# Performance work log

Measured on AMD Instinct MI355X. Metric: run time of the kernel, lower is better.

Reference implementation:

```python
import jax, jax.numpy as jnp
import numpy as np

H = 1024  # hidden_features
I = 64    # input_dims
O = 2     # output_dims
T = 4096  # timesteps


def setup_inputs() -> dict:
    key = jax.random.key(0)
    ks = jax.random.split(key, 12)
    s = 1.0 / np.sqrt(H)  # torch LSTMCell/Linear init scale
    return {
        "x_in":  jax.random.normal(ks[0], (T, I), dtype=jnp.float32),
        "W_ih1": jax.random.uniform(ks[1], (4 * H, I), jnp.float32, -s, s),
        "W_hh1": jax.random.uniform(ks[2], (4 * H, H), jnp.float32, -s, s),
        "b_ih1": jax.random.uniform(ks[3], (4 * H,), jnp.float32, -s, s),
        "b_hh1": jax.random.uniform(ks[4], (4 * H,), jnp.float32, -s, s),
        "W_ih2": jax.random.uniform(ks[5], (4 * H, H), jnp.float32, -s, s),
        "W_hh2": jax.random.uniform(ks[6], (4 * H, H), jnp.float32, -s, s),
        "b_ih2": jax.random.uniform(ks[7], (4 * H,), jnp.float32, -s, s),
        "b_hh2": jax.random.uniform(ks[8], (4 * H,), jnp.float32, -s, s),
        "W_out": jax.random.uniform(ks[9], (O, H), jnp.float32, -s, s),
        "b_out": jax.random.uniform(ks[10], (O,), jnp.float32, -s, s),
    }


def _lstm_cell(x, h, c, W_ih, W_hh, b_ih, b_hh):
    # PyTorch LSTMCell gate order: i, f, g, o
    gates = x @ W_ih.T + b_ih + h @ W_hh.T + b_hh  # [4H]
    i, f, g, o = jnp.split(gates, 4)
    i = jax.nn.sigmoid(i)
    f = jax.nn.sigmoid(f)
    g = jnp.tanh(g)
    o = jax.nn.sigmoid(o)
    c_new = f * c + i * g
    h_new = o * jnp.tanh(c_new)
    return h_new, c_new


def reference(x_in, W_ih1, W_hh1, b_ih1, b_hh1,
              W_ih2, W_hh2, b_ih2, b_hh2, W_out, b_out):
    def step(carry, x_t):
        h1, c1, h2, c2 = carry
        h1, c1 = _lstm_cell(x_t, h1, c1, W_ih1, W_hh1, b_ih1, b_hh1)
        h2, c2 = _lstm_cell(h1, h2, c2, W_ih2, W_hh2, b_ih2, b_hh2)
        out = h2 @ W_out.T + b_out  # [O]
        return (h1, c1, h2, c2), out

    z = jnp.zeros((H,), dtype=x_in.dtype)
    init = (z, z, z, z)
    _, outputs = jax.lax.scan(step, init, x_in)  # outputs: [T, O]
    return outputs
```

## Files before the change

### kernel.cpp

```cpp
#include <hip/hip_runtime.h>
#include <math.h>


#define HID 1024
#define DIN 64
#define TSTEPS 4096
#define NWG 256
#define TPB 512

typedef unsigned long long u64;
typedef unsigned int u32;

#define H2_OFF 2048
#define WS_NEED_U64 (2048ull + 4097ull * 1024ull)
#define WS_NEED_BYTES (WS_NEED_U64 * 8ull)
#define WS_ZERO_BYTES 32768

#define WLDS_F4 (16 * 512)
#define DYN_LDS_BYTES (WLDS_F4 * 16 + 2 * 1152 * 4)

__device__ __forceinline__ float sigmoid_f(float v) {
    return 1.0f / (1.0f + __expf(-v));
}
__device__ __forceinline__ float tanh_f(float v) {
    return 2.0f / (1.0f + __expf(-2.0f * v)) - 1.0f;
}

__device__ __forceinline__ void st_pair(u64* p, float h, u32 tag) {
    u64 pk = ((u64)tag << 32) | (u64)__float_as_uint(h);
    __hip_atomic_store(p, pk, __ATOMIC_RELAXED, __HIP_MEMORY_SCOPE_AGENT);
}
__device__ __forceinline__ u64 ld_pair(const u64* p) {
    return __hip_atomic_load(p, __ATOMIC_RELAXED, __HIP_MEMORY_SCOPE_AGENT);
}
#define PTAG(v) ((u32)((v) >> 32))
#define PVAL(v) (__uint_as_float((u32)(v)))

#define PIN4(v) asm volatile("" : "+v"((v).x), "+v"((v).y), "+v"((v).z), "+v"((v).w))
#define PIN_W1() do { \
    PIN4(w1a); PIN4(w1b); PIN4(w1c); PIN4(w1d); \
    PIN4(w1e); PIN4(w1f); PIN4(w1g); PIN4(w1h); \
} while (0)

#define ASTEP(j, W1) do {                                           \
    float4 hv = *(const float4*)(hb + 4*(j));                       \
    float4 w2 = wlds[(j)*512 + tid];                                \
    a0 = fmaf((W1).x, hv.x, a0); a1 = fmaf((W1).y, hv.y, a1);       \
    a2 = fmaf((W1).z, hv.z, a2); a3 = fmaf((W1).w, hv.w, a3);       \
    e0 = fmaf(w2.x, hv.x, e0); e1 = fmaf(w2.y, hv.y, e1);           \
    e2 = fmaf(w2.z, hv.z, e2); e3 = fmaf(w2.w, hv.w, e3);           \
} while (0)

#define BSTEP(j) do {                                               \
    float4 gv = *(const float4*)(gb + 4*(j));                       \
    float4 w3 = wlds[(8+(j))*512 + tid];                            \
    e0 = fmaf(w3.x, gv.x, e0); e1 = fmaf(w3.y, gv.y, e1);           \
    e2 = fmaf(w3.z, gv.z, e2); e3 = fmaf(w3.w, gv.w, e3);           \
} while (0)

__global__ void
__attribute__((amdgpu_flat_work_group_size(TPB, TPB), amdgpu_waves_per_eu(2, 2)))
lstm_persistent(
    const float* __restrict__ x,
    const float* __restrict__ Wih1, const float* __restrict__ Whh1,
    const float* __restrict__ bih1, const float* __restrict__ bhh1,
    const float* __restrict__ Wih2, const float* __restrict__ Whh2,
    const float* __restrict__ bih2, const float* __restrict__ bhh2,
    const float* __restrict__ Wout, const float* __restrict__ bout,
    float* __restrict__ out, u64* __restrict__ ws, int use_hist)
{
    const int wg   = blockIdx.x;
    const int tid  = threadIdx.x;
    const int wave = tid >> 6;
    const int lane = tid & 63;
    const int gate = tid >> 7;
    const int rsub = (tid >> 5) & 3;
    const int c    = tid & 31;
    const int row  = gate * HID + (wg << 2) + rsub;
    const int kbase = c << 5;

    u64* h1t = ws;
    u64* h2t = ws + H2_OFF;

    extern __shared__ __align__(16) char smem[];
    float4* wlds = (float4*)smem;
    float*  h1s  = (float*)(smem + WLDS_F4 * 16);
    float*  h2s  = h1s + 1152;

    {
        const float4* q2 = (const float4*)(Wih2 + (size_t)row * HID + kbase);
        const float4* q3 = (const float4*)(Whh2 + (size_t)row * HID + kbase);
        #pragma unroll
        for (int j = 0; j < 8; ++j) wlds[j * 512 + tid] = q2[j];
        #pragma unroll
        for (int j = 0; j < 8; ++j) wlds[(8 + j) * 512 + tid] = q3[j];
    }

    const float4* p1 = (const float4*)(Whh1 + (size_t)row * HID + kbase);
    float4 w1a = p1[0], w1b = p1[1], w1c = p1[2], w1d = p1[3];
    float4 w1e = p1[4], w1f = p1[5], w1g = p1[6], w1h = p1[7];
    PIN_W1();

    const float2 wx = *(const float2*)(Wih1 + (size_t)row * DIN + (c << 1));
    const float bsum1 = bih1[row] + bhh1[row];
    const float bsum2 = bih2[row] + bhh2[row];

    __shared__ float g1[4][4], g2[4][4];
    __shared__ float c1s[4], c2s[4];
    __shared__ float red0[8], red1[8];
    if (tid < 4) { c1s[tid] = 0.0f; c2s[tid] = 0.0f; }

    const int sdst = 36 * (tid >> 4) + ((tid << 1) & 31);
    const int sbase = 36 * c;

    __syncthreads();

    for (int p = 0; p <= TSTEPS; ++p) {
        const u64* h1p = h1t + (size_t)(p & 1) * 1024 + (tid << 1);
        const int h2row_c = (p > 0) ? (use_hist ? (p - 1) : ((p - 1) & 1)) : 0;
        const u64* h2p = h2t + (size_t)h2row_c * 1024 + (tid << 1);
        const u32 want1 = (u32)p;
        const u32 want2 = (p >= 2) ? (u32)p : 0u;

        const int tx = (p < TSTEPS) ? p : 0;
        const float2 xv = *(const float2*)(x + (size_t)tx * DIN + (c << 1));

        u64 v1a, v1b;
        {
            int guard = 0;
            for (;;) {
                v1a = ld_pair(h1p); v1b = ld_pair(h1p + 1);
                if ((PTAG(v1a) == want1) & (PTAG(v1b) == want1)) break;
                if (++guard > (1 << 17)) break;
            }
        }
        u64 v2a = ld_pair(h2p), v2b = ld_pair(h2p + 1);

        PIN_W1();

        *(float2*)(h1s + sdst) = make_float2(PVAL(v1a), PVAL(v1b));
        __syncthreads();

        float a0=0.f, a1=0.f, a2=0.f, a3=0.f;
        float e0=0.f, e1=0.f, e2=0.f, e3=0.f;
        const float* hb = h1s + sbase;
        ASTEP(0, w1a); ASTEP(1, w1b); ASTEP(2, w1c); ASTEP(3, w1d);
        ASTEP(4, w1e); ASTEP(5, w1f); ASTEP(6, w1g); ASTEP(7, w1h);
        a0 = fmaf(wx.x, xv.x, a0);
        a1 = fmaf(wx.y, xv.y, a1);

        float accA = (a0 + a1) + (a2 + a3);
        accA += __shfl_xor(accA, 1);
        accA += __shfl_xor(accA, 2);
        accA += __shfl_xor(accA, 4);
        accA += __shfl_xor(accA, 8);
        accA += __shfl_xor(accA, 16);
        if (c == 0) {
            float vA = accA + bsum1;
            g1[gate][rsub] = (gate == 2) ? tanh_f(vA) : sigmoid_f(vA);
        }

        {
            int guard = 0;
            while (!((PTAG(v2a) == want2) & (PTAG(v2b) == want2))) {
                v2a = ld_pair(h2p); v2b = ld_pair(h2p + 1);
                if (++guard > (1 << 17)) break;
            }
        }
        float sb0 = PVAL(v2a), sb1 = PVAL(v2b);
        *(float2*)(h2s + sdst) = make_float2(sb0, sb1);
        __syncthreads();

        if (p < TSTEPS && tid < 4) {
            float iv = g1[0][tid], fv = g1[1][tid];
            float gv = g1[2][tid], ov = g1[3][tid];
            float cn = fv * c1s[tid] + iv * gv;
            c1s[tid] = cn;
            st_pair(h1t + (size_t)((p + 1) & 1) * 1024 + (wg << 2) + tid,
                    ov * tanh_f(cn), (u32)(p + 1));
        }

        const float* gb = h2s + sbase;
        BSTEP(0); BSTEP(1); BSTEP(2); BSTEP(3);
        BSTEP(4); BSTEP(5); BSTEP(6); BSTEP(7);

        float accB = (e0 + e1) + (e2 + e3);
        accB += __shfl_xor(accB, 1);
        accB += __shfl_xor(accB, 2);
        accB += __shfl_xor(accB, 4);
        accB += __shfl_xor(accB, 8);
        accB += __shfl_xor(accB, 16);
        if (c == 0) {
            float vB = accB + bsum2;
            g2[gate][rsub] = (gate == 2) ? tanh_f(vB) : sigmoid_f(vB);
        }
        __syncthreads();

        if (p >= 1 && tid >= 4 && tid < 8) {
            int u = tid - 4;
            float iv = g2[0][u], fv = g2[1][u];
            float gv = g2[2][u], ov = g2[3][u];
            float cn = fv * c2s[u] + iv * gv;
            c2s[u] = cn;
            const int wr = use_hist ? p : (p & 1);
            st_pair(h2t + (size_t)wr * 1024 + (wg << 2) + u,
                    ov * tanh_f(cn), (u32)(p + 1));
        }

        if (!use_hist && wg == 0 && p >= 2) {
            const float2 wo0 = *(const float2*)(Wout + (tid << 1));
            const float2 wo1 = *(const float2*)(Wout + HID + (tid << 1));
            float q0 = wo0.x * sb0 + wo0.y * sb1;
            float q1 = wo1.x * sb0 + wo1.y * sb1;
            #pragma unroll
            for (int m = 1; m < 64; m <<= 1) {
                q0 += __shfl_xor(q0, m);
                q1 += __shfl_xor(q1, m);
            }
            if (lane == 0) { red0[wave] = q0; red1[wave] = q1; }
            __syncthreads();
            if (tid == 0) {
                float o0 = bout[0], o1 = bout[1];
                #pragma unroll
                for (int w = 0; w < 8; ++w) { o0 += red0[w]; o1 += red1[w]; }
                out[2*(p-2)+0] = o0;
                out[2*(p-2)+1] = o1;
            }
            __syncthreads();
        }
    }

    if (use_hist) {
        const float2 wo0 = *(const float2*)(Wout + (tid << 1));
        const float2 wo1 = *(const float2*)(Wout + HID + (tid << 1));
        const float bo0 = bout[0], bo1 = bout[1];
        for (int i = 0; i < 16; ++i) {
            const int t = (wg << 4) + i;
            const u64* hp = h2t + (size_t)(t + 1) * 1024 + (tid << 1);
            const u32 want = (u32)(t + 2);
            u64 va, vb; int guard = 0;
            for (;;) {
                va = ld_pair(hp); vb = ld_pair(hp + 1);
                if ((PTAG(va) == want) && (PTAG(vb) == want)) break;
                if (++guard > (1 << 15)) break;
            }
            float h0 = PVAL(va), h1v = PVAL(vb);
            float q0 = wo0.x * h0 + wo0.y * h1v;
            float q1 = wo1.x * h0 + wo1.y * h1v;
            #pragma unroll
            for (int m = 1; m < 64; m <<= 1) {
                q0 += __shfl_xor(q0, m);
                q1 += __shfl_xor(q1, m);
            }
            if (lane == 0) { red0[wave] = q0; red1[wave] = q1; }
            __syncthreads();
            if (tid == 0) {
                float o0 = bo0, o1 = bo1;
                #pragma unroll
                for (int w = 0; w < 8; ++w) { o0 += red0[w]; o1 += red1[w]; }
                out[2*t+0] = o0;
                out[2*t+1] = o1;
            }
            __syncthreads();
        }
    } else if (wg == 0) {
        const float2 wo0 = *(const float2*)(Wout + (tid << 1));
        const float2 wo1 = *(const float2*)(Wout + HID + (tid << 1));
        const u64* hp = h2t + (size_t)(TSTEPS & 1) * 1024 + (tid << 1);
        const u32 want = (u32)(TSTEPS + 1);
        u64 va, vb; int guard = 0;
        for (;;) {
            va = ld_pair(hp); vb = ld_pair(hp + 1);
            if ((PTAG(va) == want) && (PTAG(vb) == want)) break;
            if (++guard > (1 << 15)) break;
        }
        float h0 = PVAL(va), h1v = PVAL(vb);
        float q0 = wo0.x * h0 + wo0.y * h1v;
        float q1 = wo1.x * h0 + wo1.y * h1v;
        #pragma unroll
        for (int m = 1; m < 64; m <<= 1) {
            q0 += __shfl_xor(q0, m);
            q1 += __shfl_xor(q1, m);
        }
        if (lane == 0) { red0[wave] = q0; red1[wave] = q1; }
        __syncthreads();
        if (tid == 0) {
            float o0 = bout[0], o1 = bout[1];
            #pragma unroll
            for (int w = 0; w < 8; ++w) { o0 += red0[w]; o1 += red1[w]; }
            out[2*(TSTEPS-1)+0] = o0;
            out[2*(TSTEPS-1)+1] = o1;
        }
    }
}

extern "C" void kernel_launch(void* const* d_in, const int* in_sizes, int n_in,
                              void* d_out, int out_size, void* d_ws, size_t ws_size,
                              hipStream_t stream)
{
    const float* x    = (const float*)d_in[0];
    const float* Wih1 = (const float*)d_in[1];
    const float* Whh1 = (const float*)d_in[2];
    const float* bih1 = (const float*)d_in[3];
    const float* bhh1 = (const float*)d_in[4];
    const float* Wih2 = (const float*)d_in[5];
    const float* Whh2 = (const float*)d_in[6];
    const float* bih2 = (const float*)d_in[7];
    const float* bhh2 = (const float*)d_in[8];
    const float* Wout = (const float*)d_in[9];
    const float* bout = (const float*)d_in[10];
    float* out = (float*)d_out;
    u64*   ws  = (u64*)d_ws;

    const int use_hist = (ws_size >= WS_NEED_BYTES) ? 1 : 0;

    (void)hipFuncSetAttribute((const void*)lstm_persistent,
                              hipFuncAttributeMaxDynamicSharedMemorySize,
                              DYN_LDS_BYTES);

    hipMemsetAsync(d_ws, 0, WS_ZERO_BYTES, stream);

    hipLaunchKernelGGL(lstm_persistent, dim3(NWG), dim3(TPB), DYN_LDS_BYTES,
                       stream,
                       x, Wih1, Whh1, bih1, bhh1,
                       Wih2, Whh2, bih2, bhh2,
                       Wout, bout, out, ws, use_hist);
}
```

Measured before the change: 8.251 ms.

## Store LSTM weights and hidden states as packed fp16 and use fdot2

Result: faster. 7.475 ms (-9.4%).

```diff
diff --git a/kernel.cpp b/kernel.cpp
--- a/kernel.cpp
+++ b/kernel.cpp
@@ -10,14 +10,18 @@
 
 typedef unsigned long long u64;
 typedef unsigned int u32;
+typedef _Float16 f16x2 __attribute__((ext_vector_type(2)));
+typedef __fp16   g16x2 __attribute__((ext_vector_type(2)));
 
 #define H2_OFF 2048
 #define WS_NEED_U64 (2048ull + 4097ull * 1024ull)
 #define WS_NEED_BYTES (WS_NEED_U64 * 8ull)
 #define WS_ZERO_BYTES 32768
 
-#define WLDS_F4 (16 * 512)
-#define DYN_LDS_BYTES (WLDS_F4 * 16 + 2 * 1152 * 4)
+#define WLDS_U4 (8 * 512)
+#define H1S_OFF (WLDS_U4 * 16)
+#define H2S_OFF (H1S_OFF + 640 * 4)
+#define DYN_LDS_BYTES (H2S_OFF + 640 * 4)
 
 __device__ __forceinline__ float sigmoid_f(float v) {
     return 1.0f / (1.0f + __expf(-v));
@@ -36,26 +40,47 @@
 #define PTAG(v) ((u32)((v) >> 32))
 #define PVAL(v) (__uint_as_float((u32)(v)))
 
-#define PIN4(v) asm volatile("" : "+v"((v).x), "+v"((v).y), "+v"((v).z), "+v"((v).w))
-#define PIN_W1() do { \
-    PIN4(w1a); PIN4(w1b); PIN4(w1c); PIN4(w1d); \
-    PIN4(w1e); PIN4(w1f); PIN4(w1g); PIN4(w1h); \
+union U32H2 { u32 u; f16x2 h; g16x2 g; };
+
+__device__ __forceinline__ u32 pk2(float a, float b) {
+    U32H2 t; t.g = __builtin_amdgcn_cvt_pkrtz(a, b); return t.u;
+}
+
+#if defined(__has_builtin)
+#if __has_builtin(__builtin_amdgcn_fdot2)
+#define HAS_FDOT2 1
+#endif
+#endif
+
+__device__ __forceinline__ float dot2f(u32 a, u32 b, float c) {
+    U32H2 x, y; x.u = a; y.u = b;
+#ifdef HAS_FDOT2
+    return __builtin_amdgcn_fdot2(x.h, y.h, c, false);
+#else
+    float r = fmaf((float)x.h.x, (float)y.h.x, c);
+    return fmaf((float)x.h.y, (float)y.h.y, r);
+#endif
+}
+
+#define PIN_W1() asm volatile("" : "+v"(w1p0), "+v"(w1p1), "+v"(w1p2), \
+    "+v"(w1p3), "+v"(w1p4), "+v"(w1p5), "+v"(w1p6), "+v"(w1p7), \
+    "+v"(w1p8), "+v"(w1p9), "+v"(w1pA), "+v"(w1pB), \
+    "+v"(w1pC), "+v"(w1pD), "+v"(w1pE), "+v"(w1pF))
+
+#define ASTEP(j, P0, P1, P2, P3) do {                               \
+    uint4 hv = *(const uint4*)(h1s + hbase + 4*(j));                \
+    uint4 w2 = wlds[(j)*512 + tid];                                 \
+    a0 = dot2f(hv.x, P0, a0); a1 = dot2f(hv.y, P1, a1);             \
+    a0 = dot2f(hv.z, P2, a0); a1 = dot2f(hv.w, P3, a1);             \
+    e0 = dot2f(hv.x, w2.x, e0); e1 = dot2f(hv.y, w2.y, e1);         \
+    e0 = dot2f(hv.z, w2.z, e0); e1 = dot2f(hv.w, w2.w, e1);         \
 } while (0)
 
-#define ASTEP(j, W1) do {                                           \
-    float4 hv = *(const float4*)(hb + 4*(j));                       \
-    float4 w2 = wlds[(j)*512 + tid];                                \
-    a0 = fmaf((W1).x, hv.x, a0); a1 = fmaf((W1).y, hv.y, a1);       \
-    a2 = fmaf((W1).z, hv.z, a2); a3 = fmaf((W1).w, hv.w, a3);       \
-    e0 = fmaf(w2.x, hv.x, e0); e1 = fmaf(w2.y, hv.y, e1);           \
-    e2 = fmaf(w2.z, hv.z, e2); e3 = fmaf(w2.w, hv.w, e3);           \
-} while (0)
-
 #define BSTEP(j) do {                                               \
-    float4 gv = *(const float4*)(gb + 4*(j));                       \
-    float4 w3 = wlds[(8+(j))*512 + tid];                            \
-    e0 = fmaf(w3.x, gv.x, e0); e1 = fmaf(w3.y, gv.y, e1);           \
-    e2 = fmaf(w3.z, gv.z, e2); e3 = fmaf(w3.w, gv.w, e3);           \
+    uint4 gv = *(const uint4*)(h2s + hbase + 4*(j));                \
+    uint4 w3 = wlds[(4+(j))*512 + tid];                             \
+    e0 = dot2f(gv.x, w3.x, e0); e1 = dot2f(gv.y, w3.y, e1);         \
+    e0 = dot2f(gv.z, w3.z, e0); e1 = dot2f(gv.w, w3.w, e1);         \
 } while (0)
 
 __global__ void
@@ -83,22 +108,38 @@
     u64* h2t = ws + H2_OFF;
 
     extern __shared__ __align__(16) char smem[];
-    float4* wlds = (float4*)smem;
-    float*  h1s  = (float*)(smem + WLDS_F4 * 16);
-    float*  h2s  = h1s + 1152;
+    uint4* wlds = (uint4*)smem;
+    u32*   h1s  = (u32*)(smem + H1S_OFF);
+    u32*   h2s  = (u32*)(smem + H2S_OFF);
 
     {
         const float4* q2 = (const float4*)(Wih2 + (size_t)row * HID + kbase);
         const float4* q3 = (const float4*)(Whh2 + (size_t)row * HID + kbase);
         #pragma unroll
-        for (int j = 0; j < 8; ++j) wlds[j * 512 + tid] = q2[j];
+        for (int j = 0; j < 4; ++j) {
+            float4 qa = q2[2*j], qb = q2[2*j+1];
+            wlds[j * 512 + tid] = make_uint4(pk2(qa.x, qa.y), pk2(qa.z, qa.w),
+                                             pk2(qb.x, qb.y), pk2(qb.z, qb.w));
+        }
         #pragma unroll
-        for (int j = 0; j < 8; ++j) wlds[(8 + j) * 512 + tid] = q3[j];
+        for (int j = 0; j < 4; ++j) {
+            float4 qa = q3[2*j], qb = q3[2*j+1];
+            wlds[(4+j) * 512 + tid] = make_uint4(pk2(qa.x, qa.y), pk2(qa.z, qa.w),
+                                                 pk2(qb.x, qb.y), pk2(qb.z, qb.w));
+        }
     }
 
     const float4* p1 = (const float4*)(Whh1 + (size_t)row * HID + kbase);
-    float4 w1a = p1[0], w1b = p1[1], w1c = p1[2], w1d = p1[3];
-    float4 w1e = p1[4], w1f = p1[5], w1g = p1[6], w1h = p1[7];
+    float4 f0 = p1[0], f1 = p1[1], f2 = p1[2], f3 = p1[3];
+    float4 f4 = p1[4], f5 = p1[5], f6 = p1[6], f7 = p1[7];
+    u32 w1p0 = pk2(f0.x, f0.y), w1p1 = pk2(f0.z, f0.w);
+    u32 w1p2 = pk2(f1.x, f1.y), w1p3 = pk2(f1.z, f1.w);
+    u32 w1p4 = pk2(f2.x, f2.y), w1p5 = pk2(f2.z, f2.w);
+    u32 w1p6 = pk2(f3.x, f3.y), w1p7 = pk2(f3.z, f3.w);
+    u32 w1p8 = pk2(f4.x, f4.y), w1p9 = pk2(f4.z, f4.w);
+    u32 w1pA = pk2(f5.x, f5.y), w1pB = pk2(f5.z, f5.w);
+    u32 w1pC = pk2(f6.x, f6.y), w1pD = pk2(f6.z, f6.w);
+    u32 w1pE = pk2(f7.x, f7.y), w1pF = pk2(f7.z, f7.w);
     PIN_W1();
 
     const float2 wx = *(const float2*)(Wih1 + (size_t)row * DIN + (c << 1));
@@ -110,8 +151,8 @@
     __shared__ float red0[8], red1[8];
     if (tid < 4) { c1s[tid] = 0.0f; c2s[tid] = 0.0f; }
 
-    const int sdst = 36 * (tid >> 4) + ((tid << 1) & 31);
-    const int sbase = 36 * c;
+    const int sdst = 20 * (tid >> 4) + (tid & 15);
+    const int hbase = 20 * c;
 
     __syncthreads();
 
@@ -138,18 +179,18 @@
 
         PIN_W1();
 
-        *(float2*)(h1s + sdst) = make_float2(PVAL(v1a), PVAL(v1b));
+        h1s[sdst] = pk2(PVAL(v1a), PVAL(v1b));
         __syncthreads();
 
-        float a0=0.f, a1=0.f, a2=0.f, a3=0.f;
-        float e0=0.f, e1=0.f, e2=0.f, e3=0.f;
-        const float* hb = h1s + sbase;
-        ASTEP(0, w1a); ASTEP(1, w1b); ASTEP(2, w1c); ASTEP(3, w1d);
-        ASTEP(4, w1e); ASTEP(5, w1f); ASTEP(6, w1g); ASTEP(7, w1h);
+        float a0 = 0.f, a1 = 0.f, e0 = 0.f, e1 = 0.f;
+        ASTEP(0, w1p0, w1p1, w1p2, w1p3);
+        ASTEP(1, w1p4, w1p5, w1p6, w1p7);
+        ASTEP(2, w1p8, w1p9, w1pA, w1pB);
+        ASTEP(3, w1pC, w1pD, w1pE, w1pF);
         a0 = fmaf(wx.x, xv.x, a0);
         a1 = fmaf(wx.y, xv.y, a1);
 
-        float accA = (a0 + a1) + (a2 + a3);
+        float accA = a0 + a1;
         accA += __shfl_xor(accA, 1);
         accA += __shfl_xor(accA, 2);
         accA += __shfl_xor(accA, 4);
@@ -168,7 +209,7 @@
             }
         }
         float sb0 = PVAL(v2a), sb1 = PVAL(v2b);
-        *(float2*)(h2s + sdst) = make_float2(sb0, sb1);
+        h2s[sdst] = pk2(sb0, sb1);
         __syncthreads();
 
         if (p < TSTEPS && tid < 4) {
@@ -180,11 +221,9 @@
                     ov * tanh_f(cn), (u32)(p + 1));
         }
 
-        const float* gb = h2s + sbase;
         BSTEP(0); BSTEP(1); BSTEP(2); BSTEP(3);
-        BSTEP(4); BSTEP(5); BSTEP(6); BSTEP(7);
-
-        float accB = (e0 + e1) + (e2 + e3);
+
+        float accB = e0 + e1;
         accB += __shfl_xor(accB, 1);
         accB += __shfl_xor(accB, 2);
         accB += __shfl_xor(accB, 4);
@@ -318,7 +357,7 @@
                               hipFuncAttributeMaxDynamicSharedMemorySize,
                               DYN_LDS_BYTES);
 
-    hipMemsetAsync(d_ws, 0, WS_ZERO_BYTES, stream);
+    (void)hipMemsetAsync(d_ws, 0, WS_ZERO_BYTES, stream);
 
     hipLaunchKernelGGL(lstm_persistent, dim3(NWG), dim3(TPB), DYN_LDS_BYTES,
                        stream,
```
